# Performance work log

Hardware: AMD Instinct MI355X
Metric: run time of the kernel (lower is better)

The kernel has to match this reference:

```python
import jax, jax.numpy as jnp
import numpy as np

N_WIRES = 3  # state vector of 2^3 = 8 amplitudes, kept as [B,2,2,2]


def _rx(t):
    c = jnp.cos(t / 2); s = jnp.sin(t / 2)
    return jnp.stack([jnp.stack([c + 0j, -1j * s], -1),
                      jnp.stack([-1j * s, c + 0j], -1)], -2).astype(jnp.complex64)


def _ry(t):
    c = jnp.cos(t / 2); s = jnp.sin(t / 2)
    return jnp.stack([jnp.stack([c, -s], -1),
                      jnp.stack([s, c], -1)], -2).astype(jnp.complex64)


def _rz(t):
    e = jnp.exp(-1j * t / 2).astype(jnp.complex64)
    z = jnp.zeros_like(e)
    return jnp.stack([jnp.stack([e, z], -1),
                      jnp.stack([z, jnp.conj(e)], -1)], -2)


def apply_1q(state, mat, wire):
    # state: [B,2,2,2]; mat: [2,2] (shared) or [B,2,2] (per-sample)
    s = jnp.moveaxis(state, 1 + wire, 1)
    sh = s.shape
    s = s.reshape(sh[0], 2, -1)
    m = jnp.broadcast_to(mat, (sh[0], 2, 2))
    s = jnp.einsum('bij,bjk->bik', m, s)
    return jnp.moveaxis(s.reshape(sh), 1, 1 + wire)


def apply_crx(state, t, ctrl, tgt):
    # controlled-RX: apply rx(t) to target subspace where control bit == 1
    mat = _rx(t)  # [2,2]
    s = jnp.moveaxis(state, (1 + ctrl, 1 + tgt), (1, 2))  # [B,2(ctrl),2(tgt),2]
    s1 = s[:, 1]                       # [B,2,2]
    sh = s1.shape
    s1 = jnp.einsum('ij,bjk->bik', mat, s1.reshape(sh[0], 2, -1)).reshape(sh)
    s = jnp.stack([s[:, 0], s1], 1)
    return jnp.moveaxis(s, (1, 2), (1 + ctrl, 1 + tgt))


def _quantum_forward(x, theta, W1, b1, W2, b2):
    B = x.shape[0]
    state = jnp.zeros((B, 2, 2, 2), jnp.complex64).at[:, 0, 0, 0].set(1.0)
    # GeneralEncoder: rx(x0)@w0, ry(x1)@w1, rz(x2)@w2
    state = apply_1q(state, _rx(x[:, 0]), 0)
    state = apply_1q(state, _ry(x[:, 1]), 1)
    state = apply_1q(state, _rz(x[:, 2]), 2)
    # RandomLayer(n_ops=8): fixed representative 8-op trainable sequence
    state = apply_1q(state, _rx(theta[0]), 0)
    state = apply_1q(state, _ry(theta[1]), 1)
    state = apply_1q(state, _rz(theta[2]), 2)
    state = apply_crx(state, theta[3], 0, 1)
    state = apply_1q(state, _ry(theta[4]), 2)
    state = apply_1q(state, _rx(theta[5]), 1)
    state = apply_crx(state, theta[6], 1, 2)
    state = apply_1q(state, _rz(theta[7]), 0)
    # measurement -> 8 basis-state probabilities (matches Linear(8,32) head)
    probs = (state.real ** 2 + state.imag ** 2).reshape(B, 8)
    h = jax.nn.relu(probs @ W1 + b1)
    return h @ W2 + b2


def setup_inputs() -> dict:
    key = jax.random.key(0)
    ks = jax.random.split(key, 6)
    B = 2_000_000
    x = jax.random.normal(ks[0], (B, 3), jnp.float32)
    theta = jax.random.normal(ks[1], (8,), jnp.float32)
    W1 = jax.random.normal(ks[2], (8, 32), jnp.float32) * 0.35   # ~1/sqrt(8)
    b1 = jnp.zeros((32,), jnp.float32)
    W2 = jax.random.normal(ks[3], (32, 2), jnp.float32) * 0.18   # ~1/sqrt(32)
    b2 = jnp.zeros((2,), jnp.float32)
    return {"x": x, "theta": theta, "W1": W1, "b1": b1, "W2": W2, "b2": b2}


def reference(x, theta, W1, b1, W2, b2):
    return _quantum_forward(x, theta, W1, b1, W2, b2)
```

## Files before the change

kernel.cpp:

```cpp
#include <hip/hip_runtime.h>


typedef float f32x2 __attribute__((ext_vector_type(2)));

static __device__ __forceinline__ f32x2 pkfma_s(f32x2 coef_s, f32x2 b, f32x2 c) {
    f32x2 d;
    asm("v_pk_fma_f32 %0, %1, %2, %3" : "=v"(d) : "s"(coef_s), "v"(b), "v"(c));
    return d;
}
static __device__ __forceinline__ f32x2 pkmul(f32x2 a, f32x2 b) {
    f32x2 d;
    asm("v_pk_mul_f32 %0, %1, %2" : "=v"(d) : "v"(a), "v"(b));
    return d;
}
static __device__ __forceinline__ f32x2 splat2(float v) {
    f32x2 r; r.x = v; r.y = v; return r;
}

#define INV_2PI 0.15915494309189535f

__global__ __launch_bounds__(64) void q_precompute(
    const float* __restrict__ theta,
    const float* __restrict__ W1,
    const float* __restrict__ b1,
    const float* __restrict__ W2,
    const float* __restrict__ b2,
    float* __restrict__ tab)
{
    __shared__ float Ure[8][8];
    __shared__ float Uim[8][8];
    const int t = threadIdx.x;

    if (t < 8) {
        float cr[8], ci[8];
        #pragma unroll
        for (int r = 0; r < 8; ++r) { cr[r] = (r == t) ? 1.f : 0.f; ci[r] = 0.f; }

        auto rxmix = [&](int a, int b, float c_, float s_) {
            float ar = cr[a], ai = ci[a], br = cr[b], bi = ci[b];
            cr[a] = c_*ar + s_*bi;   ci[a] = c_*ai - s_*br;
            cr[b] = s_*ai + c_*br;   ci[b] = -s_*ar + c_*bi;
        };
        auto rymix = [&](int a, int b, float c_, float s_) {
            float ar = cr[a], ai = ci[a], br = cr[b], bi = ci[b];
            cr[a] = c_*ar - s_*br;   ci[a] = c_*ai - s_*bi;
            cr[b] = s_*ar + c_*br;   ci[b] = s_*ai + c_*bi;
        };
        auto zmul = [&](int r, float u, float v) {
            float xr = cr[r], xi = ci[r];
            cr[r] = xr*u - xi*v;  ci[r] = xr*v + xi*u;
        };
        auto hsin = [&](float a) { return __builtin_amdgcn_sinf(a * (0.5f*INV_2PI)); };
        auto hcos = [&](float a) { return __builtin_amdgcn_cosf(a * (0.5f*INV_2PI)); };

        float c, s;
        c = hcos(theta[0]); s = hsin(theta[0]);
        rxmix(0,4,c,s); rxmix(1,5,c,s); rxmix(2,6,c,s); rxmix(3,7,c,s);
        c = hcos(theta[1]); s = hsin(theta[1]);
        rymix(0,2,c,s); rymix(1,3,c,s); rymix(4,6,c,s); rymix(5,7,c,s);
        c = hcos(theta[2]); s = hsin(theta[2]);
        #pragma unroll
        for (int r = 0; r < 8; ++r) zmul(r, c, (r & 1) ? s : -s);
        c = hcos(theta[3]); s = hsin(theta[3]);
        rxmix(4,6,c,s); rxmix(5,7,c,s);
        c = hcos(theta[4]); s = hsin(theta[4]);
        rymix(0,1,c,s); rymix(2,3,c,s); rymix(4,5,c,s); rymix(6,7,c,s);
        c = hcos(theta[5]); s = hsin(theta[5]);
        rxmix(0,2,c,s); rxmix(1,3,c,s); rxmix(4,6,c,s); rxmix(5,7,c,s);
        c = hcos(theta[6]); s = hsin(theta[6]);
        rxmix(2,3,c,s); rxmix(6,7,c,s);
        c = hcos(theta[7]); s = hsin(theta[7]);
        #pragma unroll
        for (int r = 0; r < 8; ++r) zmul(r, c, (r < 4) ? -s : s);

        #pragma unroll
        for (int r = 0; r < 8; ++r) { Ure[r][t] = cr[r]; Uim[r][t] = ci[r]; }
    }
    __syncthreads();

    if (t < 32) {
        float Wre[8][4], Wim[8][4];
        #pragma unroll
        for (int j = 0; j < 8; ++j) {
            Wre[j][0] =  Ure[j][0]; Wim[j][0] =  Uim[j][0];
            Wre[j][1] =  Ure[j][2]; Wim[j][1] =  Uim[j][2];
            Wre[j][2] =  Uim[j][4]; Wim[j][2] = -Ure[j][4];
            Wre[j][3] =  Uim[j][6]; Wim[j][3] = -Ure[j][6];
        }
        float Q[4][4];
        #pragma unroll
        for (int m = 0; m < 4; ++m)
            #pragma unroll
            for (int n = 0; n < 4; ++n) Q[m][n] = 0.f;
        #pragma unroll
        for (int j = 0; j < 8; ++j) {
            float w = W1[j*32 + t];
            #pragma unroll
            for (int m = 0; m < 4; ++m)
                #pragma unroll
                for (int n = 0; n < 4; ++n)
                    Q[m][n] = fmaf(w, Wre[j][m]*Wre[j][n] + Wim[j][m]*Wim[j][n], Q[m][n]);
        }
        float R[3][3];
        R[0][0] = Q[0][0];
        R[0][1] = Q[0][1] + Q[1][0];
        R[0][2] = Q[1][1];
        R[1][0] = Q[0][2] + Q[2][0];
        R[1][1] = Q[0][3] + Q[1][2] + Q[2][1] + Q[3][0];
        R[1][2] = Q[1][3] + Q[3][1];
        R[2][0] = Q[2][2];
        R[2][1] = Q[2][3] + Q[3][2];
        R[2][2] = Q[3][3];
        float P[3][3];
        #pragma unroll
        for (int b = 0; b < 3; ++b) {
            P[0][b] = 0.5f*(R[0][b] + R[2][b]);
            P[1][b] = 0.5f*(R[0][b] - R[2][b]);
            P[2][b] = 0.5f*R[1][b];
        }
        float T[3][3];
        #pragma unroll
        for (int si = 0; si < 3; ++si) {
            T[si][0] = 0.5f*(P[si][0] + P[si][2]);
            T[si][1] = 0.5f*(P[si][0] - P[si][2]);
            T[si][2] = 0.5f*P[si][1];
        }
        float* row = tab + t*24;
        row[0]  = row[1]  = T[0][1];
        row[2]  = row[3]  = T[0][2];
        row[4]  = row[5]  = T[1][0];
        row[6]  = row[7]  = T[2][0];
        row[8]  = row[9]  = T[1][1];
        row[10] = row[11] = T[1][2];
        row[12] = row[13] = T[2][1];
        row[14] = row[15] = T[2][2];
        row[16] = row[17] = b1[t] + T[0][0];
        row[18] = row[19] = W2[t*2+0];
        row[20] = row[21] = W2[t*2+1];
        row[22] = row[23] = 0.f;
    }
    if (t == 0) { tab[768] = b2[0]; tab[769] = b2[1]; }
}

__global__ __launch_bounds__(256) void q_main(
    const float* __restrict__ x,
    const float* __restrict__ tab,
    float* __restrict__ out,
    int B)
{
    const int lid = threadIdx.x;
    const int bb  = blockIdx.x * 2048;
    const int e0  = bb + lid;

    const float b2a = tab[768], b2b = tab[769];
    const f32x2* Tp = reinterpret_cast<const f32x2*>(tab);

    float xs0[8], xs1[8];
    #pragma unroll
    for (int k = 0; k < 8; ++k) {
        int e = e0 + k*256;
        e = (e < B) ? e : (B - 1);
        xs0[k] = x[e*3 + 0];
        xs1[k] = x[e*3 + 1];
    }

    f32x2 c0v[4], s0v[4], c1v[4], s1v[4], pcc[4], pcs[4], psc[4], pss[4];
    #pragma unroll
    for (int g = 0; g < 4; ++g) {
        #pragma unroll
        for (int j = 0; j < 2; ++j) {
            const int k = 2*g + j;
            const float r0 = xs0[k] * INV_2PI;
            const float r1 = xs1[k] * INV_2PI;
            s0v[g][j] = __builtin_amdgcn_sinf(r0);
            c0v[g][j] = __builtin_amdgcn_cosf(r0);
            s1v[g][j] = __builtin_amdgcn_sinf(r1);
            c1v[g][j] = __builtin_amdgcn_cosf(r1);
        }
        pcc[g] = pkmul(c0v[g], c1v[g]);
        pcs[g] = pkmul(c0v[g], s1v[g]);
        psc[g] = pkmul(s0v[g], c1v[g]);
        pss[g] = pkmul(s0v[g], s1v[g]);
    }

    f32x2 a0v[4], a1v[4];
    #pragma unroll
    for (int g = 0; g < 4; ++g) { a0v[g] = splat2(b2a); a1v[g] = splat2(b2b); }
    const f32x2 zero2 = splat2(0.f);

    #pragma unroll 2
    for (int l = 0; l < 32; ++l) {
        const int L = l*12;
        const f32x2 cT01 = Tp[L+0];
        const f32x2 cT02 = Tp[L+1];
        const f32x2 cT10 = Tp[L+2];
        const f32x2 cT20 = Tp[L+3];
        const f32x2 cT11 = Tp[L+4];
        const f32x2 cT12 = Tp[L+5];
        const f32x2 cT21 = Tp[L+6];
        const f32x2 cT22 = Tp[L+7];
        const f32x2 cw0  = Tp[L+9];
        const f32x2 cw1  = Tp[L+10];
        const f32x2 vb   = splat2(tab[l*24 + 16]);
        #pragma unroll
        for (int g = 0; g < 4; ++g) {
            f32x2 h = pkfma_s(cT01, c1v[g], vb);
            h = pkfma_s(cT02, s1v[g], h);
            h = pkfma_s(cT10, c0v[g], h);
            h = pkfma_s(cT20, s0v[g], h);
            h = pkfma_s(cT11, pcc[g], h);
            h = pkfma_s(cT12, pcs[g], h);
            h = pkfma_s(cT21, psc[g], h);
            h = pkfma_s(cT22, pss[g], h);
            h = __builtin_elementwise_max(h, zero2);
            a0v[g] = pkfma_s(cw0, h, a0v[g]);
            a1v[g] = pkfma_s(cw1, h, a1v[g]);
        }
    }

    f32x2* O2 = (f32x2*)out;
    #pragma unroll
    for (int k = 0; k < 8; ++k) {
        const int e = e0 + k*256;
        if (e < B) {
            f32x2 o; o.x = a0v[k>>1][k&1]; o.y = a1v[k>>1][k&1];
            O2[e] = o;
        }
    }
}

extern "C" void kernel_launch(void* const* d_in, const int* in_sizes, int n_in,
                              void* d_out, int out_size, void* d_ws, size_t ws_size,
                              hipStream_t stream) {
    const float* x     = (const float*)d_in[0];
    const float* theta = (const float*)d_in[1];
    const float* W1    = (const float*)d_in[2];
    const float* b1    = (const float*)d_in[3];
    const float* W2    = (const float*)d_in[4];
    const float* b2    = (const float*)d_in[5];
    float* out = (float*)d_out;
    float* tab = (float*)d_ws;

    const int B = in_sizes[0] / 3;

    q_precompute<<<1, 64, 0, stream>>>(theta, W1, b1, W2, b2, tab);

    const int blocks = (B + 2047) / 2048;
    q_main<<<blocks, 256, 0, stream>>>(x, tab, out, B);
}
```

Measured before the change: 98.50 us.

## Fuse parameter precompute into main kernel with per-block LDS table

```diff
diff --git a/kernel.cpp b/kernel.cpp
--- a/kernel.cpp
+++ b/kernel.cpp
@@ -3,9 +3,9 @@
 
 typedef float f32x2 __attribute__((ext_vector_type(2)));
 
-static __device__ __forceinline__ f32x2 pkfma_s(f32x2 coef_s, f32x2 b, f32x2 c) {
+static __device__ __forceinline__ f32x2 pkfma(f32x2 a, f32x2 b, f32x2 c) {
     f32x2 d;
-    asm("v_pk_fma_f32 %0, %1, %2, %3" : "=v"(d) : "s"(coef_s), "v"(b), "v"(c));
+    asm("v_pk_fma_f32 %0, %1, %2, %3" : "=v"(d) : "v"(a), "v"(b), "v"(c));
     return d;
 }
 static __device__ __forceinline__ f32x2 pkmul(f32x2 a, f32x2 b) {
@@ -19,17 +19,32 @@
 
 #define INV_2PI 0.15915494309189535f
 
-__global__ __launch_bounds__(64) void q_precompute(
+__global__ __launch_bounds__(256) void q_fused(
+    const float* __restrict__ x,
     const float* __restrict__ theta,
     const float* __restrict__ W1,
     const float* __restrict__ b1,
     const float* __restrict__ W2,
     const float* __restrict__ b2,
-    float* __restrict__ tab)
+    float* __restrict__ out,
+    int B)
 {
     __shared__ float Ure[8][8];
     __shared__ float Uim[8][8];
-    const int t = threadIdx.x;
+    __shared__ __align__(16) float tabL[32*24 + 4];
+
+    const int t  = threadIdx.x;
+    const int bb = blockIdx.x * 2048;
+    const int e0 = bb + t;
+
+    float xs0[8], xs1[8];
+    #pragma unroll
+    for (int k = 0; k < 8; ++k) {
+        int e = e0 + k*256;
+        e = (e < B) ? e : (B - 1);
+        xs0[k] = x[e*3 + 0];
+        xs1[k] = x[e*3 + 1];
+    }
 
     if (t < 8) {
         float cr[8], ci[8];
@@ -125,7 +140,7 @@
             T[si][1] = 0.5f*(P[si][0] - P[si][2]);
             T[si][2] = 0.5f*P[si][1];
         }
-        float* row = tab + t*24;
+        float* row = tabL + t*24;
         row[0]  = row[1]  = T[0][1];
         row[2]  = row[3]  = T[0][2];
         row[4]  = row[5]  = T[1][0];
@@ -139,30 +154,7 @@
         row[20] = row[21] = W2[t*2+1];
         row[22] = row[23] = 0.f;
     }
-    if (t == 0) { tab[768] = b2[0]; tab[769] = b2[1]; }
-}
-
-__global__ __launch_bounds__(256) void q_main(
-    const float* __restrict__ x,
-    const float* __restrict__ tab,
-    float* __restrict__ out,
-    int B)
-{
-    const int lid = threadIdx.x;
-    const int bb  = blockIdx.x * 2048;
-    const int e0  = bb + lid;
-
-    const float b2a = tab[768], b2b = tab[769];
-    const f32x2* Tp = reinterpret_cast<const f32x2*>(tab);
-
-    float xs0[8], xs1[8];
-    #pragma unroll
-    for (int k = 0; k < 8; ++k) {
-        int e = e0 + k*256;
-        e = (e < B) ? e : (B - 1);
-        xs0[k] = x[e*3 + 0];
-        xs1[k] = x[e*3 + 1];
-    }
+    if (t == 0) { tabL[768] = b2[0]; tabL[769] = b2[1]; }
 
     f32x2 c0v[4], s0v[4], c1v[4], s1v[4], pcc[4], pcs[4], psc[4], pss[4];
     #pragma unroll
@@ -182,12 +174,15 @@
         psc[g] = pkmul(s0v[g], c1v[g]);
         pss[g] = pkmul(s0v[g], s1v[g]);
     }
-
+    __syncthreads();
+
+    const float b2a = tabL[768], b2b = tabL[769];
     f32x2 a0v[4], a1v[4];
     #pragma unroll
     for (int g = 0; g < 4; ++g) { a0v[g] = splat2(b2a); a1v[g] = splat2(b2b); }
     const f32x2 zero2 = splat2(0.f);
 
+    const f32x2* Tp = reinterpret_cast<const f32x2*>(tabL);
     #pragma unroll 2
     for (int l = 0; l < 32; ++l) {
         const int L = l*12;
@@ -199,22 +194,22 @@
         const f32x2 cT12 = Tp[L+5];
         const f32x2 cT21 = Tp[L+6];
         const f32x2 cT22 = Tp[L+7];
+        const f32x2 vb   = Tp[L+8];
         const f32x2 cw0  = Tp[L+9];
         const f32x2 cw1  = Tp[L+10];
-        const f32x2 vb   = splat2(tab[l*24 + 16]);
         #pragma unroll
         for (int g = 0; g < 4; ++g) {
-            f32x2 h = pkfma_s(cT01, c1v[g], vb);
-            h = pkfma_s(cT02, s1v[g], h);
-            h = pkfma_s(cT10, c0v[g], h);
-            h = pkfma_s(cT20, s0v[g], h);
-            h = pkfma_s(cT11, pcc[g], h);
-            h = pkfma_s(cT12, pcs[g], h);
-            h = pkfma_s(cT21, psc[g], h);
-            h = pkfma_s(cT22, pss[g], h);
+            f32x2 h = pkfma(cT01, c1v[g], vb);
+            h = pkfma(cT02, s1v[g], h);
+            h = pkfma(cT10, c0v[g], h);
+            h = pkfma(cT20, s0v[g], h);
+            h = pkfma(cT11, pcc[g], h);
+            h = pkfma(cT12, pcs[g], h);
+            h = pkfma(cT21, psc[g], h);
+            h = pkfma(cT22, pss[g], h);
             h = __builtin_elementwise_max(h, zero2);
-            a0v[g] = pkfma_s(cw0, h, a0v[g]);
-            a1v[g] = pkfma_s(cw1, h, a1v[g]);
+            a0v[g] = pkfma(cw0, h, a0v[g]);
+            a1v[g] = pkfma(cw1, h, a1v[g]);
         }
     }
 
@@ -239,12 +234,9 @@
     const float* W2    = (const float*)d_in[4];
     const float* b2    = (const float*)d_in[5];
     float* out = (float*)d_out;
-    float* tab = (float*)d_ws;
+    (void)d_ws; (void)ws_size;
 
     const int B = in_sizes[0] / 3;
-
-    q_precompute<<<1, 64, 0, stream>>>(theta, W1, b1, W2, b2, tab);
-
     const int blocks = (B + 2047) / 2048;
-    q_main<<<blocks, 256, 0, stream>>>(x, tab, out, B);
-}
+    q_fused<<<blocks, 256, 0, stream>>>(x, theta, W1, b1, W2, b2, out, B);
+}
```

After: 100.1 us. No clear change (+1.6%).
